# Kernel optimization log

Hardware: AMD Instinct MI355X
Metric: run time of the kernel (lower is better)

Reference implementation:

```python
import jax, jax.numpy as jnp
import numpy as np


def setup_inputs() -> dict:
    key = jax.random.key(0)
    k1, k2 = jax.random.split(key)
    B, C, T = 32, 384, 1024
    x = jax.random.normal(k1, (B, C, T), dtype=jnp.float32)
    duration = jax.random.randint(k2, (B, T), 0, 8, dtype=jnp.int32)
    return {"x": x, "duration": duration, "max_len": 7168}


def reference(x, duration, max_len):
    # x: [B, C, T], duration: [B, T] int32
    # Vectorized equivalent of per-phoneme repeat_interleave + pad.
    csum = jnp.cumsum(duration, axis=1)              # [B, T] exclusive-right boundaries
    mel_len = csum[:, -1]                            # [B] total expanded length
    frames = jnp.arange(max_len, dtype=jnp.int32)    # [L]
    # phoneme index owning each output frame: searchsorted skips zero-duration phonemes
    idx = jax.vmap(lambda c: jnp.searchsorted(c, frames, side='right'))(csum)  # [B, L]
    idx = jnp.clip(idx, 0, x.shape[2] - 1)
    out = jnp.take_along_axis(x, idx[:, None, :], axis=2)  # [B, C, L] gather along T
    valid = frames[None, :] < mel_len[:, None]              # [B, L] padding mask
    out = jnp.where(valid[:, None, :], out, jnp.zeros((), dtype=x.dtype))
    return out, mel_len.astype(jnp.int32)
```

## Files before the change

kernel.cpp:

```cpp
#include <hip/hip_runtime.h>


#define B_ 32
#define C_ 384
#define T_ 1024
#define MAXLEN_ 7168
#define FT_ 7
#define CPB_ 4
#define NT_ 256
#define NCG_ (C_ / CPB_)
#define NWG_ (FT_ * NCG_ * B_)
#define NXCD_ 8

typedef float f32x4 __attribute__((ext_vector_type(4)));

__global__ __launch_bounds__(NT_) void lr_fused_kernel(
    const int* __restrict__ dur,
    const float* __restrict__ x,
    float* __restrict__ out,
    float* __restrict__ mel_out)
{
    const int tid = threadIdx.x;

    const int bid  = blockIdx.x;
    const int wgid = (bid & (NXCD_ - 1)) * (NWG_ / NXCD_) + (bid >> 3);
    const int ftile = wgid % FT_;
    const int rest  = wgid / FT_;
    const int cblk  = rest % NCG_;
    const int b     = rest / NCG_;
    const int f0    = ftile << 10;

    __shared__ float s_x[CPB_][T_];
    __shared__ unsigned short s_map[1024];
    __shared__ int s_w[NT_ / 64];

    const int4 d4 = ((const int4*)(dur + b * T_))[tid];
    const int sum4 = d4.x + d4.y + d4.z + d4.w;

    const int lane = tid & 63;
    const int wave = tid >> 6;
    int sc = sum4;
    #pragma unroll
    for (int d = 1; d < 64; d <<= 1) {
        int n = __shfl_up(sc, d, 64);
        if (lane >= d) sc += n;
    }
    if (lane == 63) s_w[wave] = sc;

    ((int2*)s_map)[tid] = make_int2(-1, -1);
    __syncthreads();

    int woff = 0;
    #pragma unroll
    for (int w = 0; w < NT_ / 64; ++w)
        woff += (w < wave) ? s_w[w] : 0;
    const int mel = s_w[0] + s_w[1] + s_w[2] + s_w[3];

    if (ftile == 0 && cblk == 0 && tid == 0)
        mel_out[b] = (float)mel;

    float* ob = out + ((size_t)b * C_ + cblk * CPB_) * MAXLEN_ + f0 + (tid << 2);

    if (f0 >= mel) {
        const f32x4 z = {0.0f, 0.0f, 0.0f, 0.0f};
        #pragma unroll
        for (int cc = 0; cc < CPB_; ++cc)
            __builtin_nontemporal_store(z, (f32x4*)(ob + (size_t)cc * MAXLEN_));
        return;
    }

    const float* xb = x + ((size_t)b * C_ + cblk * CPB_) * T_;
    #pragma unroll
    for (int r = 0; r < CPB_; ++r)
        ((f32x4*)s_x[r])[tid] = ((const f32x4*)(xb + r * T_))[tid];

    {
        const int st = woff + sc - sum4;
        const int base_tok = tid << 2;
        const int s0 = st;
        const int s1 = s0 + d4.x;
        const int s2 = s1 + d4.y;
        const int s3 = s2 + d4.z;
        const int starts[4] = { s0, s1, s2, s3 };
        const int lens[4]   = { d4.x, d4.y, d4.z, d4.w };
        #pragma unroll
        for (int k = 0; k < 4; ++k) {
            int lo = starts[k] - f0;
            int hi = lo + lens[k];
            lo = lo < 0 ? 0 : lo;
            hi = hi > 1024 ? 1024 : hi;
            for (int p = lo; p < hi; ++p)
                s_map[p] = (unsigned short)(base_tok + k);
        }
    }
    __syncthreads();

    const uint2 m = ((const uint2*)s_map)[tid];
    const unsigned int t0 = m.x & 0xFFFFu, t1 = m.x >> 16;
    const unsigned int t2 = m.y & 0xFFFFu, t3 = m.y >> 16;

    #pragma unroll
    for (int cc = 0; cc < CPB_; ++cc) {
        const float a0 = s_x[cc][t0 & 1023u];
        const float a1 = s_x[cc][t1 & 1023u];
        const float a2 = s_x[cc][t2 & 1023u];
        const float a3 = s_x[cc][t3 & 1023u];
        f32x4 v;
        v.x = (t0 <= 1023u) ? a0 : 0.0f;
        v.y = (t1 <= 1023u) ? a1 : 0.0f;
        v.z = (t2 <= 1023u) ? a2 : 0.0f;
        v.w = (t3 <= 1023u) ? a3 : 0.0f;
        __builtin_nontemporal_store(v, (f32x4*)(ob + (size_t)cc * MAXLEN_));
    }
}

extern "C" void kernel_launch(void* const* d_in, const int* in_sizes, int n_in,
                              void* d_out, int out_size, void* d_ws, size_t ws_size,
                              hipStream_t stream) {
    const float* x   = (const float*)d_in[0];
    const int*   dur = (const int*)d_in[1];

    float* out = (float*)d_out;
    float* mel_out = out + (size_t)B_ * C_ * MAXLEN_;

    lr_fused_kernel<<<NWG_, NT_, 0, stream>>>(dur, x, out, mel_out);
}
```

Baseline: 67.38 us.

## Split duration prefix-scan into separate kernel and reuse cumsum in gather

Moves the per-batch cumulative sum of durations into a small scan kernel that writes boundaries and mel length to workspace. The gather kernel then reads the precomputed boundaries instead of redoing a block-wide scan in every workgroup, and it masks padding by comparing against mel rather than with a sentinel map. This trades redundant per-block scan work and a barrier for an extra kernel launch and a global round trip through workspace.

```diff
diff --git a/kernel.cpp b/kernel.cpp
--- a/kernel.cpp
+++ b/kernel.cpp
@@ -11,27 +11,17 @@
 #define NCG_ (C_ / CPB_)
 #define NWG_ (FT_ * NCG_ * B_)
 #define NXCD_ 8
+#define CSTRIDE_ 1028
 
 typedef float f32x4 __attribute__((ext_vector_type(4)));
 
-__global__ __launch_bounds__(NT_) void lr_fused_kernel(
+__global__ __launch_bounds__(NT_) void lr_scan_kernel(
     const int* __restrict__ dur,
-    const float* __restrict__ x,
-    float* __restrict__ out,
+    int* __restrict__ csum,
     float* __restrict__ mel_out)
 {
+    const int b = blockIdx.x;
     const int tid = threadIdx.x;
-
-    const int bid  = blockIdx.x;
-    const int wgid = (bid & (NXCD_ - 1)) * (NWG_ / NXCD_) + (bid >> 3);
-    const int ftile = wgid % FT_;
-    const int rest  = wgid / FT_;
-    const int cblk  = rest % NCG_;
-    const int b     = rest / NCG_;
-    const int f0    = ftile << 10;
-
-    __shared__ float s_x[CPB_][T_];
-    __shared__ unsigned short s_map[1024];
     __shared__ int s_w[NT_ / 64];
 
     const int4 d4 = ((const int4*)(dur + b * T_))[tid];
@@ -46,18 +36,44 @@
         if (lane >= d) sc += n;
     }
     if (lane == 63) s_w[wave] = sc;
-
-    ((int2*)s_map)[tid] = make_int2(-1, -1);
     __syncthreads();
 
     int woff = 0;
     #pragma unroll
     for (int w = 0; w < NT_ / 64; ++w)
         woff += (w < wave) ? s_w[w] : 0;
-    const int mel = s_w[0] + s_w[1] + s_w[2] + s_w[3];
 
-    if (ftile == 0 && cblk == 0 && tid == 0)
+    const int e0 = woff + sc - sum4;
+    int4 e;
+    e.x = e0;
+    e.y = e0 + d4.x;
+    e.z = e.y + d4.y;
+    e.w = e.z + d4.z;
+    ((int4*)(csum + b * CSTRIDE_))[tid] = e;
+
+    if (tid == NT_ - 1) {
+        const int mel = e.w + d4.w;
+        csum[b * CSTRIDE_ + T_] = mel;
         mel_out[b] = (float)mel;
+    }
+}
+
+__global__ __launch_bounds__(NT_) void lr_gather_kernel(
+    const int* __restrict__ csum,
+    const float* __restrict__ x,
+    float* __restrict__ out)
+{
+    const int tid = threadIdx.x;
+
+    const int bid  = blockIdx.x;
+    const int wgid = (bid & (NXCD_ - 1)) * (NWG_ / NXCD_) + (bid >> 3);
+    const int ftile = wgid % FT_;
+    const int rest  = wgid / FT_;
+    const int cblk  = rest % NCG_;
+    const int b     = rest / NCG_;
+    const int f0    = ftile << 10;
+
+    const int mel = csum[b * CSTRIDE_ + T_];
 
     float* ob = out + ((size_t)b * C_ + cblk * CPB_) * MAXLEN_ + f0 + (tid << 2);
 
@@ -69,24 +85,25 @@
         return;
     }
 
+    __shared__ float s_x[CPB_][T_];
+    __shared__ unsigned short s_map[1024];
+
     const float* xb = x + ((size_t)b * C_ + cblk * CPB_) * T_;
     #pragma unroll
     for (int r = 0; r < CPB_; ++r)
         ((f32x4*)s_x[r])[tid] = ((const f32x4*)(xb + r * T_))[tid];
 
-    {
-        const int st = woff + sc - sum4;
+    const int4 e = ((const int4*)(csum + b * CSTRIDE_))[tid];
+    const int e4 = csum[b * CSTRIDE_ + (tid << 2) + 4];
+
+    if (e.x < f0 + 1024 && e4 > f0) {
         const int base_tok = tid << 2;
-        const int s0 = st;
-        const int s1 = s0 + d4.x;
-        const int s2 = s1 + d4.y;
-        const int s3 = s2 + d4.z;
-        const int starts[4] = { s0, s1, s2, s3 };
-        const int lens[4]   = { d4.x, d4.y, d4.z, d4.w };
+        const int starts[4] = { e.x, e.y, e.z, e.w };
+        const int ends[4]   = { e.y, e.z, e.w, e4 };
         #pragma unroll
         for (int k = 0; k < 4; ++k) {
             int lo = starts[k] - f0;
-            int hi = lo + lens[k];
+            int hi = ends[k] - f0;
             lo = lo < 0 ? 0 : lo;
             hi = hi > 1024 ? 1024 : hi;
             for (int p = lo; p < hi; ++p)
@@ -96,20 +113,19 @@
     __syncthreads();
 
     const uint2 m = ((const uint2*)s_map)[tid];
-    const unsigned int t0 = m.x & 0xFFFFu, t1 = m.x >> 16;
-    const unsigned int t2 = m.y & 0xFFFFu, t3 = m.y >> 16;
+    const unsigned int t0 = m.x & 1023u, t1 = (m.x >> 16) & 1023u;
+    const unsigned int t2 = m.y & 1023u, t3 = (m.y >> 16) & 1023u;
+    const int f = f0 + (tid << 2);
+    const bool v0 = (f + 0) < mel, v1 = (f + 1) < mel;
+    const bool v2 = (f + 2) < mel, v3 = (f + 3) < mel;
 
     #pragma unroll
     for (int cc = 0; cc < CPB_; ++cc) {
-        const float a0 = s_x[cc][t0 & 1023u];
-        const float a1 = s_x[cc][t1 & 1023u];
-        const float a2 = s_x[cc][t2 & 1023u];
-        const float a3 = s_x[cc][t3 & 1023u];
         f32x4 v;
-        v.x = (t0 <= 1023u) ? a0 : 0.0f;
-        v.y = (t1 <= 1023u) ? a1 : 0.0f;
-        v.z = (t2 <= 1023u) ? a2 : 0.0f;
-        v.w = (t3 <= 1023u) ? a3 : 0.0f;
+        v.x = v0 ? s_x[cc][t0] : 0.0f;
+        v.y = v1 ? s_x[cc][t1] : 0.0f;
+        v.z = v2 ? s_x[cc][t2] : 0.0f;
+        v.w = v3 ? s_x[cc][t3] : 0.0f;
         __builtin_nontemporal_store(v, (f32x4*)(ob + (size_t)cc * MAXLEN_));
     }
 }
@@ -122,6 +138,8 @@
 
     float* out = (float*)d_out;
     float* mel_out = out + (size_t)B_ * C_ * MAXLEN_;
+    int* csum = (int*)d_ws;
 
-    lr_fused_kernel<<<NWG_, NT_, 0, stream>>>(dur, x, out, mel_out);
+    lr_scan_kernel<<<B_, NT_, 0, stream>>>(dur, csum, mel_out);
+    lr_gather_kernel<<<NWG_, NT_, 0, stream>>>(csum, x, out);
 }
```

Result: slower. 73.13 us (+8.5%).
